# Performance work log

Measured on AMD Instinct MI355X. Metric: run time of the kernel, lower is better.

Reference implementation:

```python
import jax, jax.numpy as jnp
import numpy as np

HIDDEN = 1000
IN_DIM = 1024


def setup_inputs() -> dict:
    key = jax.random.key(0)
    ks = jax.random.split(key, 9)
    s = 0.05
    return {
        "x": jax.random.normal(ks[0], (64, 128, IN_DIM), dtype=jnp.float32),
        "W1": jax.random.normal(ks[1], (IN_DIM, 4 * HIDDEN), dtype=jnp.float32) * s,
        "U1": jax.random.normal(ks[2], (HIDDEN, 4 * HIDDEN), dtype=jnp.float32) * s,
        "b1": jnp.zeros((4 * HIDDEN,), dtype=jnp.float32),
        "W2": jax.random.normal(ks[3], (HIDDEN, 4 * HIDDEN), dtype=jnp.float32) * s,
        "U2": jax.random.normal(ks[4], (HIDDEN, 4 * HIDDEN), dtype=jnp.float32) * s,
        "b2": jnp.zeros((4 * HIDDEN,), dtype=jnp.float32),
        "Wo": jax.random.normal(ks[5], (HIDDEN, 6), dtype=jnp.float32) * s,
        "bo": jnp.zeros((6,), dtype=jnp.float32),
    }


def _lstm_step(h, c, z):
    # Keras LSTMCell gate order: i, f, g(cell), o
    i, f, g, o = jnp.split(z, 4, axis=-1)
    i = jax.nn.sigmoid(i)
    f = jax.nn.sigmoid(f)
    o = jax.nn.sigmoid(o)
    c_new = f * c + i * jnp.tanh(g)
    h_new = o * jnp.tanh(c_new)
    return h_new, c_new


def reference(x, W1, U1, b1, W2, U2, b2, Wo, bo):
    B = x.shape[0]
    xs = jnp.swapaxes(x, 0, 1)  # [T, B, D]

    def step(carry, xt):
        h1, c1, h2, c2 = carry
        z1 = xt @ W1 + h1 @ U1 + b1
        h1, c1 = _lstm_step(h1, c1, z1)
        z2 = h1 @ W2 + h2 @ U2 + b2
        h2, c2 = _lstm_step(h2, c2, z2)
        return (h1, c1, h2, c2), None

    zeros = jnp.zeros((B, HIDDEN), dtype=x.dtype)
    (h1, c1, h2, c2), _ = jax.lax.scan(step, (zeros, zeros, zeros, zeros), xs)
    # RNN(return_sequences=False) returns last top-cell hidden state
    return h2 @ Wo + bo
```

## Files before the change

kernel.cpp:

```cpp
#include <hip/hip_runtime.h>
#include <hip/hip_bf16.h>

#define TT 128
#define DD 1024
#define HH 1000
#define NBLK 252
#define RING 16

typedef float f32x4 __attribute__((ext_vector_type(4)));
typedef __bf16 bf16x8 __attribute__((ext_vector_type(8)));

__device__ __forceinline__ bf16x8 asbf(f32x4 v) { return __builtin_bit_cast(bf16x8, v); }

__device__ __forceinline__ void ld_a(bf16x8* d, const char* p) {
    asm volatile("global_load_dwordx4 %0, %1, off sc0" : "=v"(*d) : "v"(p));
}
__device__ __forceinline__ void st_h32(char* p, unsigned v) {
    asm volatile("global_store_dword %0, %1, off sc0 sc1" :: "v"(p), "v"(v) : "memory");
}
__device__ __forceinline__ void st_ctl(unsigned* p, unsigned v) {
    asm volatile("global_store_dword %0, %1, off sc0 sc1" :: "v"(p), "v"(v) : "memory");
}

#define AT_RLX __ATOMIC_RELAXED
#define SC_AGT __HIP_MEMORY_SCOPE_AGENT

__global__ void zero_sel(char* __restrict__ ws) {
    int i = blockIdx.x * 256 + threadIdx.x;
    if (i >= 67584) return;
    unsigned* p;
    if (i < 32768)      p = (unsigned*)(ws + (size_t)15 * 131072) + i;
    else if (i < 65536) p = (unsigned*)(ws + (size_t)31 * 131072) + (i - 32768);
    else                p = (unsigned*)(ws + (size_t)32 * 131072) + (i - 65536);
    *p = 0u;
}

__global__ void cast_x(const float* __restrict__ x, __bf16* __restrict__ xfh) {
    int gid = blockIdx.x * 256 + threadIdx.x;
    int lane = gid & 63;
    int mt = (gid >> 6) & 3;
    int ks = (gid >> 8) & 31;
    int t  = gid >> 13;
    int row = mt * 16 + (lane & 15);
    int k0  = ks * 32 + (lane >> 4) * 8;
    const float* sp = x + ((size_t)row * TT + t) * 1024 + k0;
    float4 v0 = *(const float4*)sp;
    float4 v1 = *(const float4*)(sp + 4);
    float f[8] = {v0.x, v0.y, v0.z, v0.w, v1.x, v1.y, v1.z, v1.w};
    bf16x8 hv;
#pragma unroll
    for (int j = 0; j < 8; ++j) hv[j] = (__bf16)f[j];
    ((bf16x8*)xfh)[gid] = hv;
}

__global__ __launch_bounds__(256) void pack_w3(
    const float* __restrict__ W1, const float* __restrict__ U1,
    const float* __restrict__ W2, const float* __restrict__ U2,
    __bf16* __restrict__ w1h, __bf16* __restrict__ w2h)
{
    int kb = blockIdx.x;
    int layer = blockIdx.y;
    const float* R1 = layer ? W2 : W1;
    const float* R2 = layer ? U2 : U1;
    int k1v = layer ? HH : 1024;
    __bf16* dh = layer ? w2h : w1h;
    int tid = threadIdx.x;

    const float* src = (kb < 128) ? R1 : R2;
    const int kmax = (kb < 128) ? k1v : HH;
    const int base = (kb & 127) * 8;

    __shared__ float lt[8][4008];

#pragma unroll 1
    for (int r = 0; r < 8; ++r) {
        bool valid = (base + r) < kmax;
        const float* rp = src + (size_t)(base + r) * 4000;
        for (int c4 = tid; c4 < 1000; c4 += 256) {
            float4 v = valid ? *(const float4*)(rp + c4 * 4)
                             : (float4){0.f, 0.f, 0.f, 0.f};
            lt[r][c4 * 4 + 0] = v.x; lt[r][c4 * 4 + 1] = v.y;
            lt[r][c4 * 4 + 2] = v.z; lt[r][c4 * 4 + 3] = v.w;
        }
    }
    __syncthreads();

    for (int u = tid; u < 4000; u += 256) {
        int nt = u >> 4, col = u & 15;
        int scol = (col & 3) * 1000 + nt * 4 + (col >> 2);
        bf16x8 hv;
#pragma unroll
        for (int j = 0; j < 8; ++j) hv[j] = (__bf16)lt[j][scol];
        size_t unit = ((size_t)nt * 256 + kb) * 16 + col;
        ((bf16x8*)dh)[unit] = hv;
    }
}

__global__ __launch_bounds__(256, 1) void lstm_persist(
    const __bf16* __restrict__ xfh,
    const __bf16* __restrict__ w1h, const __bf16* __restrict__ w2h,
    const float* __restrict__ b1, const float* __restrict__ b2,
    __bf16* hbuf, unsigned int* ctrl)
{
    unsigned* xcdm    = ctrl + 32;
    unsigned* xcdFlag = ctrl + 384;
    unsigned* arr     = ctrl + 512;

    const int bid = blockIdx.x;
    const int layer = bid >= 126;
    const int r0 = layer ? bid - 126 : bid;
    const int bh = r0 >= 63;
    const int nb = bh ? r0 - 63 : r0;
    const int tid = threadIdx.x;
    const int lane = tid & 63, w = tid >> 6;
    const int op = w >> 1, kh = w & 1;
    const int ln = lane & 15, kg = lane >> 4;

    const char* h1ring = (const char*)hbuf;
    const char* h2ring = (const char*)(hbuf + (size_t)RING * 65536);

    __shared__ unsigned s_ldr;
    if (tid == 0) {
        unsigned x;
        asm volatile("s_getreg_b32 %0, hwreg(HW_REG_XCC_ID)" : "=s"(x));
        x &= 7u;
        unsigned old = __hip_atomic_fetch_add(&xcdm[x], 1u, AT_RLX, SC_AGT);
        s_ldr = (x << 8) | (old == 0u ? 1u : 0u);
    }

    const f32x4* wfh = (const f32x4*)(layer ? w2h : w1h);
    f32x4 WH[64];
#pragma unroll
    for (int tl = 0; tl < 4; ++tl) {
        int nt = nb * 4 + tl; if (nt > 249) nt = 249;
#pragma unroll
        for (int ks = 0; ks < 16; ++ks) {
            int kb = op * 128 + kh * 64 + ks * 4 + kg;
            WH[tl * 16 + ks] = wfh[((size_t)nt * 256 + kb) * 16 + ln];
        }
    }
#define PIN8(p0,p1,p2,p3,p4,p5,p6,p7) \
    asm volatile("" : "+a"(p0),"+a"(p1),"+a"(p2),"+a"(p3),"+a"(p4),"+a"(p5),"+a"(p6),"+a"(p7))
    PIN8(WH[0],WH[1],WH[2],WH[3],WH[4],WH[5],WH[6],WH[7]);
    PIN8(WH[8],WH[9],WH[10],WH[11],WH[12],WH[13],WH[14],WH[15]);
    PIN8(WH[16],WH[17],WH[18],WH[19],WH[20],WH[21],WH[22],WH[23]);
    PIN8(WH[24],WH[25],WH[26],WH[27],WH[28],WH[29],WH[30],WH[31]);
    PIN8(WH[32],WH[33],WH[34],WH[35],WH[36],WH[37],WH[38],WH[39]);
    PIN8(WH[40],WH[41],WH[42],WH[43],WH[44],WH[45],WH[46],WH[47]);
    PIN8(WH[48],WH[49],WH[50],WH[51],WH[52],WH[53],WH[54],WH[55]);
    PIN8(WH[56],WH[57],WH[58],WH[59],WH[60],WH[61],WH[62],WH[63]);
#undef PIN8

    const float* bias = layer ? b2 : b1;
    const int gb = tid >> 3;
    const int gcl0 = (tid * 2) & 15;
    float bias_q[2][4];
#pragma unroll
    for (int q = 0; q < 2; ++q) {
        int n = nb * 16 + gcl0 + q; if (n > HH - 1) n = HH - 1;
#pragma unroll
        for (int g = 0; g < 4; ++g) bias_q[q][g] = bias[(size_t)g * HH + n];
    }
    float creg[2] = {0.f, 0.f};

    __shared__ float zs[4][32][68];
    __syncthreads();

#pragma unroll 1
    for (int t = 0; t <= TT; ++t) {
        const bool active = layer ? (t >= 1) : (t <= TT - 1);
        if (active) {
            const char *pAh;
            char *poh;
            if (layer == 0) {
                if (op == 0) pAh = (const char*)xfh + (size_t)t * 131072;
                else         pAh = h1ring + (size_t)((t - 1) & (RING - 1)) * 131072;
                poh = (char*)(h1ring + (size_t)(t & (RING - 1)) * 131072);
            } else {
                if (op == 0) pAh = h1ring + (size_t)((t - 1) & (RING - 1)) * 131072;
                else         pAh = h2ring + (size_t)((t - 2) & (RING - 1)) * 131072;
                poh = (char*)(h2ring + (size_t)((t - 1) & (RING - 1)) * 131072);
            }
            pAh += ((size_t)kh * 4096 + bh * 128 + lane) * 16;

            f32x4 acc[4][2];
#pragma unroll
            for (int tl = 0; tl < 4; ++tl)
#pragma unroll
                for (int mt = 0; mt < 2; ++mt) acc[tl][mt] = (f32x4){0.f, 0.f, 0.f, 0.f};

            bf16x8 rh[8][2];
#define LDB(s, k) do { _Pragma("unroll") \
    for (int mt = 0; mt < 2; ++mt) \
        ld_a(&rh[s][mt], pAh + (size_t)((k) * 256 + mt * 64) * 16); \
    } while (0)
#define CPK(k, s) do { _Pragma("unroll") \
    for (int tl = 0; tl < 4; ++tl) { \
        bf16x8 wh_ = asbf(WH[tl * 16 + (k)]); \
        _Pragma("unroll") \
        for (int mt = 0; mt < 2; ++mt) \
            acc[tl][mt] = __builtin_amdgcn_mfma_f32_16x16x32_bf16(rh[s][mt], wh_, acc[tl][mt], 0, 0, 0); \
    } } while (0)

            LDB(0, 0); LDB(1, 1); LDB(2, 2); LDB(3, 3);
            LDB(4, 4); LDB(5, 5); LDB(6, 6); LDB(7, 7);
#pragma unroll
            for (int ks = 0; ks < 16; ++ks) {
                if (ks <= 8)       asm volatile("s_waitcnt vmcnt(14)" ::: "memory");
                else if (ks == 9)  asm volatile("s_waitcnt vmcnt(12)" ::: "memory");
                else if (ks == 10) asm volatile("s_waitcnt vmcnt(10)" ::: "memory");
                else if (ks == 11) asm volatile("s_waitcnt vmcnt(8)"  ::: "memory");
                else if (ks == 12) asm volatile("s_waitcnt vmcnt(6)"  ::: "memory");
                else if (ks == 13) asm volatile("s_waitcnt vmcnt(4)"  ::: "memory");
                else if (ks == 14) asm volatile("s_waitcnt vmcnt(2)"  ::: "memory");
                else               asm volatile("s_waitcnt vmcnt(0)"  ::: "memory");
                __builtin_amdgcn_sched_barrier(0);
                CPK(ks, ks & 7);
                if (ks < 8) LDB(ks & 7, ks + 8);
            }
#undef LDB
#undef CPK

#pragma unroll
            for (int tl = 0; tl < 4; ++tl)
#pragma unroll
                for (int mt = 0; mt < 2; ++mt)
#pragma unroll
                    for (int r = 0; r < 4; ++r)
                        zs[w][mt * 16 + kg * 4 + r][tl * 16 + ln] = acc[tl][mt][r];
            __syncthreads();

            {
                int cc = (gcl0 >> 2) * 16 + (gcl0 & 3) * 4;
                float hv2[2];
#pragma unroll
                for (int q = 0; q < 2; ++q) {
                    float zg[4];
#pragma unroll
                    for (int g = 0; g < 4; ++g)
                        zg[g] = zs[0][gb][cc + q * 4 + g] + zs[1][gb][cc + q * 4 + g]
                              + zs[2][gb][cc + q * 4 + g] + zs[3][gb][cc + q * 4 + g]
                              + bias_q[q][g];
                    float ig = 1.f / (1.f + __expf(-zg[0]));
                    float fg = 1.f / (1.f + __expf(-zg[1]));
                    float gg = 1.f - 2.f / (__expf(2.f * zg[2]) + 1.f);
                    float og = 1.f / (1.f + __expf(-zg[3]));
                    float cn = fg * creg[q] + ig * gg;
                    creg[q] = cn;
                    hv2[q] = og * (1.f - 2.f / (__expf(2.f * cn) + 1.f));
                }
                if (nb * 16 + gcl0 < HH) {
                    unsigned pk = (unsigned)__builtin_bit_cast(unsigned short, (__bf16)hv2[0])
                                | ((unsigned)__builtin_bit_cast(unsigned short, (__bf16)hv2[1]) << 16);
                    int mt_l = gb >> 4, lnn = gb & 15;
                    int kgsel = gcl0 >> 3, j0 = gcl0 & 7;
                    size_t unit = (((size_t)(nb >> 1) * 4 + bh * 2 + mt_l) * 64)
                                + ((nb & 1) * 2 + kgsel) * 16 + lnn;
                    st_h32(poh + unit * 16 + (size_t)j0 * 2, pk);
                }
            }
            asm volatile("s_waitcnt vmcnt(0)" ::: "memory");
        }

        if (t < TT) {
            __syncthreads();
            const unsigned tp1 = (unsigned)(t + 1);
            if (w == 0) {
                if (tid == 0) st_ctl(arr + (size_t)bid * 4, tp1);
                const unsigned* a0 = arr + (size_t)lane * 4;
                bool done = false;
                while (!done) {
                    unsigned v0, v1, v2, v3;
                    asm volatile("global_load_dword %0, %1, off sc0 sc1" : "=v"(v0) : "v"(a0));
                    asm volatile("global_load_dword %0, %1, off sc0 sc1" : "=v"(v1) : "v"(a0 + 256));
                    asm volatile("global_load_dword %0, %1, off sc0 sc1" : "=v"(v2) : "v"(a0 + 512));
                    asm volatile("global_load_dword %0, %1, off sc0 sc1" : "=v"(v3) : "v"(a0 + 768));
                    asm volatile("s_waitcnt vmcnt(0)" ::: "memory");
                    bool ok = (v0 >= tp1) && (v1 >= tp1) && (v2 >= tp1)
                           && ((lane + 192 >= NBLK) || (v3 >= tp1));
                    done = __all(ok);
                    if (!done) __builtin_amdgcn_s_sleep(1);
                }
                if ((tp1 & (RING - 1u)) == 0u) {
                    if (tid == 0) {
                        unsigned info = s_ldr;
                        unsigned* fP = xcdFlag + (info >> 8) * 16;
                        if (info & 1u) {
                            __builtin_amdgcn_fence(__ATOMIC_ACQUIRE, "agent");
                            asm volatile("s_waitcnt vmcnt(0) lgkmcnt(0)" ::: "memory");
                            __hip_atomic_store(fP, tp1, AT_RLX, SC_AGT);
                        } else {
                            while (__hip_atomic_load(fP, AT_RLX, SC_AGT) < tp1)
                                __builtin_amdgcn_s_sleep(1);
                        }
                    }
                    __builtin_amdgcn_wave_barrier();
                }
            }
            __syncthreads();
        }
    }
}

__global__ void out_proj(const __bf16* __restrict__ h2h,
                         const float* __restrict__ Wo, const float* __restrict__ bo,
                         float* __restrict__ out)
{
    int b = blockIdx.x, tid = threadIdx.x;
    int mt = b >> 4, ln = b & 15;
    float acc[6] = {0, 0, 0, 0, 0, 0};
    for (int n = tid; n < HH; n += 256) {
        int ks = n >> 5, kg = (n >> 3) & 3, j = n & 7;
        size_t idx = (((size_t)ks * 4 + mt) * 64 + kg * 16 + ln) * 8 + j;
        float h = (float)h2h[idx];
#pragma unroll
        for (int o = 0; o < 6; ++o) acc[o] += h * Wo[n * 6 + o];
    }
#pragma unroll
    for (int o = 0; o < 6; ++o)
        for (int off = 32; off; off >>= 1) acc[o] += __shfl_down(acc[o], off, 64);
    __shared__ float red[4][6];
    int lane = tid & 63, wv = tid >> 6;
    if (lane == 0) {
#pragma unroll
        for (int o = 0; o < 6; ++o) red[wv][o] = acc[o];
    }
    __syncthreads();
    if (tid < 6) {
        float s = bo[tid];
#pragma unroll
        for (int w = 0; w < 4; ++w) s += red[w][tid];
        out[b * 6 + tid] = s;
    }
}

extern "C" void kernel_launch(void* const* d_in, const int* in_sizes, int n_in,
                              void* d_out, int out_size, void* d_ws, size_t ws_size,
                              hipStream_t stream) {
    const float* x  = (const float*)d_in[0];
    const float* W1 = (const float*)d_in[1];
    const float* U1 = (const float*)d_in[2];
    const float* b1 = (const float*)d_in[3];
    const float* W2 = (const float*)d_in[4];
    const float* U2 = (const float*)d_in[5];
    const float* b2 = (const float*)d_in[6];
    const float* Wo = (const float*)d_in[7];
    const float* bo = (const float*)d_in[8];
    float* out = (float*)d_out;

    char* p = (char*)d_ws;
    __bf16* hbuf = (__bf16*)p; p += (size_t)2 * RING * 65536 * 2;
    unsigned int* ctrl = (unsigned int*)p; p += 8192;
    __bf16* xfh = (__bf16*)p; p += (size_t)8388608 * 2;
    __bf16* w1h = (__bf16*)p; p += (size_t)8192000 * 2;
    __bf16* w2h = (__bf16*)p; p += (size_t)8192000 * 2;

    zero_sel<<<264, 256, 0, stream>>>((char*)d_ws);
    cast_x<<<4096, 256, 0, stream>>>(x, xfh);
    pack_w3<<<dim3(256, 2), 256, 0, stream>>>(W1, U1, W2, U2, w1h, w2h);

    lstm_persist<<<NBLK, 256, 0, stream>>>(xfh, w1h, w2h, b1, b2, hbuf, ctrl);

    out_proj<<<64, 256, 0, stream>>>(hbuf + (size_t)(RING + 15) * 65536, Wo, bo, out);
}
```

Before: 665.8 us.

## Enlarge hidden-state ring to full sequence and pack arrival flags contiguously

The hidden-state ring grows from 16 to 128 slots, so every timestep writes to a fresh buffer. That removes the periodic per-XCD leader election, acquire fence and flag wait that guarded against stale cached data when ring slots were reused. Arrival counters are now packed one dword per block, so each polling lane reads four flags with a single dwordx4 load instead of four strided loads. The cost is a much larger workspace footprint, and correctness now relies on never reusing an address within a call.

Measured after the change: 882.9 us. 1.33x slower.

```diff
diff --git a/kernel.cpp b/kernel.cpp
--- a/kernel.cpp
+++ b/kernel.cpp
@@ -5,10 +5,11 @@
 #define DD 1024
 #define HH 1000
 #define NBLK 252
-#define RING 16
+#define RING 128
 
 typedef float f32x4 __attribute__((ext_vector_type(4)));
 typedef __bf16 bf16x8 __attribute__((ext_vector_type(8)));
+typedef unsigned u32x4 __attribute__((ext_vector_type(4)));
 
 __device__ __forceinline__ bf16x8 asbf(f32x4 v) { return __builtin_bit_cast(bf16x8, v); }
 
@@ -29,9 +30,9 @@
     int i = blockIdx.x * 256 + threadIdx.x;
     if (i >= 67584) return;
     unsigned* p;
-    if (i < 32768)      p = (unsigned*)(ws + (size_t)15 * 131072) + i;
-    else if (i < 65536) p = (unsigned*)(ws + (size_t)31 * 131072) + (i - 32768);
-    else                p = (unsigned*)(ws + (size_t)32 * 131072) + (i - 65536);
+    if (i < 32768)      p = (unsigned*)(ws + (size_t)127 * 131072) + i;
+    else if (i < 65536) p = (unsigned*)(ws + (size_t)255 * 131072) + (i - 32768);
+    else                p = (unsigned*)(ws + (size_t)256 * 131072) + (i - 65536);
     *p = 0u;
 }
 
@@ -102,9 +103,7 @@
     const float* __restrict__ b1, const float* __restrict__ b2,
     __bf16* hbuf, unsigned int* ctrl)
 {
-    unsigned* xcdm    = ctrl + 32;
-    unsigned* xcdFlag = ctrl + 384;
-    unsigned* arr     = ctrl + 512;
+    unsigned* arr = ctrl + 512;
 
     const int bid = blockIdx.x;
     const int layer = bid >= 126;
@@ -118,15 +117,6 @@
 
     const char* h1ring = (const char*)hbuf;
     const char* h2ring = (const char*)(hbuf + (size_t)RING * 65536);
-
-    __shared__ unsigned s_ldr;
-    if (tid == 0) {
-        unsigned x;
-        asm volatile("s_getreg_b32 %0, hwreg(HW_REG_XCC_ID)" : "=s"(x));
-        x &= 7u;
-        unsigned old = __hip_atomic_fetch_add(&xcdm[x], 1u, AT_RLX, SC_AGT);
-        s_ldr = (x << 8) | (old == 0u ? 1u : 0u);
-    }
 
     const f32x4* wfh = (const f32x4*)(layer ? w2h : w1h);
     f32x4 WH[64];
@@ -164,7 +154,6 @@
     float creg[2] = {0.f, 0.f};
 
     __shared__ float zs[4][32][68];
-    __syncthreads();
 
 #pragma unroll 1
     for (int t = 0; t <= TT; ++t) {
@@ -266,35 +255,19 @@
             __syncthreads();
             const unsigned tp1 = (unsigned)(t + 1);
             if (w == 0) {
-                if (tid == 0) st_ctl(arr + (size_t)bid * 4, tp1);
-                const unsigned* a0 = arr + (size_t)lane * 4;
+                if (tid == 0) st_ctl(arr + bid, tp1);
+                const unsigned* a0 = arr + lane * 4;
+                const bool l_all = (lane * 4 + 3) < NBLK;
                 bool done = false;
                 while (!done) {
-                    unsigned v0, v1, v2, v3;
-                    asm volatile("global_load_dword %0, %1, off sc0 sc1" : "=v"(v0) : "v"(a0));
-                    asm volatile("global_load_dword %0, %1, off sc0 sc1" : "=v"(v1) : "v"(a0 + 256));
-                    asm volatile("global_load_dword %0, %1, off sc0 sc1" : "=v"(v2) : "v"(a0 + 512));
-                    asm volatile("global_load_dword %0, %1, off sc0 sc1" : "=v"(v3) : "v"(a0 + 768));
+                    u32x4 v;
+                    asm volatile("global_load_dwordx4 %0, %1, off sc0 sc1"
+                                 : "=v"(v) : "v"(a0));
                     asm volatile("s_waitcnt vmcnt(0)" ::: "memory");
-                    bool ok = (v0 >= tp1) && (v1 >= tp1) && (v2 >= tp1)
-                           && ((lane + 192 >= NBLK) || (v3 >= tp1));
+                    bool ok = !l_all || ((v[0] >= tp1) && (v[1] >= tp1)
+                                      && (v[2] >= tp1) && (v[3] >= tp1));
                     done = __all(ok);
                     if (!done) __builtin_amdgcn_s_sleep(1);
-                }
-                if ((tp1 & (RING - 1u)) == 0u) {
-                    if (tid == 0) {
-                        unsigned info = s_ldr;
-                        unsigned* fP = xcdFlag + (info >> 8) * 16;
-                        if (info & 1u) {
-                            __builtin_amdgcn_fence(__ATOMIC_ACQUIRE, "agent");
-                            asm volatile("s_waitcnt vmcnt(0) lgkmcnt(0)" ::: "memory");
-                            __hip_atomic_store(fP, tp1, AT_RLX, SC_AGT);
-                        } else {
-                            while (__hip_atomic_load(fP, AT_RLX, SC_AGT) < tp1)
-                                __builtin_amdgcn_s_sleep(1);
-                        }
-                    }
-                    __builtin_amdgcn_wave_barrier();
                 }
             }
             __syncthreads();
@@ -361,5 +334,5 @@
 
     lstm_persist<<<NBLK, 256, 0, stream>>>(xfh, w1h, w2h, b1, b2, hbuf, ctrl);
 
-    out_proj<<<64, 256, 0, stream>>>(hbuf + (size_t)(RING + 15) * 65536, Wo, bo, out);
-}
+    out_proj<<<64, 256, 0, stream>>>(hbuf + (size_t)(RING + 127) * 65536, Wo, bo, out);
+}
```
